# Kernel optimization log

Measured on AMD Instinct MI355X. Metric: run time of the kernel, lower is better.

## Reference

```python
import jax, jax.numpy as jnp
import numpy as np

B, T, C = 2, 2048, 768
H, N_LEFT = 12, 6
D = C // H


def setup_inputs() -> dict:
    key = jax.random.key(0)
    ks = jax.random.split(key, 4)
    x = jax.random.normal(ks[0], (B, T, C), dtype=jnp.float32)
    attention_mask = jnp.ones((B, T), dtype=jnp.int32)
    Wqkv_w = jax.random.normal(ks[1], (3 * C, C), dtype=jnp.float32) * (C ** -0.5)
    Wqkv_b = jnp.zeros((3 * C,), dtype=jnp.float32)
    Wo_w = jax.random.normal(ks[2], (C, C), dtype=jnp.float32) * (C ** -0.5)
    Wo_b = jnp.zeros((C,), dtype=jnp.float32)
    return {"x": x, "attention_mask": attention_mask, "Wqkv_w": Wqkv_w,
            "Wqkv_b": Wqkv_b, "Wo_w": Wo_w, "Wo_b": Wo_b}


def _attend(q, k, v, mask):
    # q,k,v: [B,h,T,D]; mask: [B,1,T,T] additive
    s = jnp.einsum('bhqd,bhkd->bhqk', q, k) * (D ** -0.5) + mask
    a = jax.nn.softmax(s.astype(jnp.float32), axis=-1).astype(q.dtype)
    return jnp.einsum('bhqk,bhkd->bhqd', a, v)


def reference(x, attention_mask, Wqkv_w, Wqkv_b, Wo_w, Wo_b):
    neg = jnp.finfo(x.dtype).min
    # padding mask [B,1,1,T]: 0 where valid, neg where padded
    pad = (1.0 - attention_mask.astype(x.dtype))[:, None, None, :] * neg
    i = jnp.arange(T)
    tri = (i[None, :] > i[:, None]).astype(x.dtype) * neg   # triu(neg, 1)
    left_mask = tri[None, None] + pad                        # causal (look left)
    right_mask = tri.T[None, None] + pad                     # anti-causal (look right)

    qkv = (x @ Wqkv_w.T + Wqkv_b).reshape(B, T, 3, H, D)
    qkv = jnp.transpose(qkv, (0, 3, 2, 1, 4))                # [B,H,3,T,D]
    q, k, v = qkv[:, :, 0], qkv[:, :, 1], qkv[:, :, 2]

    lc = _attend(q[:, :N_LEFT], k[:, :N_LEFT], v[:, :N_LEFT], left_mask)
    rc = _attend(q[:, N_LEFT:], k[:, N_LEFT:], v[:, N_LEFT:], right_mask)
    ctx = jnp.concatenate([lc, rc], axis=1)                  # [B,H,T,D]
    ctx = jnp.transpose(ctx, (0, 2, 1, 3)).reshape(B, T, C)
    out = ctx @ Wo_w.T + Wo_b
    return out
```

## Files before the change

### kernel.cpp

```cpp
#include <hip/hip_runtime.h>


typedef unsigned short u16;
typedef __bf16 bf16x8 __attribute__((ext_vector_type(8)));
typedef float fx4 __attribute__((ext_vector_type(4)));
typedef unsigned short u16x8 __attribute__((ext_vector_type(8)));
typedef unsigned short u16x4 __attribute__((ext_vector_type(4)));
typedef _Float16 hx4 __attribute__((ext_vector_type(4)));
typedef __fp16 fp16x2 __attribute__((ext_vector_type(2)));

#define T_SEQ 2048
#define C_DIM 768
#define NHEAD 12
#define HDIM  64
#define NCHUNK 1152
#define NHEAVY 384
#define LOG2E_8 0.18033688f

__device__ __forceinline__ u16 f2bf(float f) {
  unsigned u = __float_as_uint(f);
  u += 0x7fffu + ((u >> 16) & 1u);
  return (u16)(u >> 16);
}
__device__ __forceinline__ u16 f2h(float f) {
  union { _Float16 h; u16 u; } cv; cv.h = (_Float16)f; return cv.u;
}

__device__ __forceinline__ void gl2lds16(const u16* g, u16* l) {
  __builtin_amdgcn_global_load_lds(
      (const __attribute__((address_space(1))) void*)g,
      (__attribute__((address_space(3))) void*)l, 16, 0, 0);
}

__global__ void cvt_swz_k(const float* __restrict__ x,
                          const float* __restrict__ wqkv,
                          const float* __restrict__ wo,
                          u16* __restrict__ out) {
  int i = blockIdx.x * blockDim.x + threadIdx.x;
  if (i >= 688128) return;
  int m = i / 96;
  int c8 = (i - m * 96) << 3;
  const float* src;
  if (m < 4096)       src = x    + (size_t)m * C_DIM + c8;
  else if (m < 6400)  src = wqkv + (size_t)(m - 4096) * C_DIM + c8;
  else                src = wo   + (size_t)(m - 6400) * C_DIM + c8;
  fx4 a = *(const fx4*)src, b = *(const fx4*)(src + 4);
  u16x8 o;
  #pragma unroll
  for (int j = 0; j < 4; ++j) { o[j] = f2bf(a[j]); o[4 + j] = f2bf(b[j]); }
  *(u16x8*)&out[(size_t)m * C_DIM + (c8 ^ ((m & 7) << 3))] = o;
}

__global__ void maskcvt_k(const int* __restrict__ am, float* __restrict__ mf,
                          unsigned* __restrict__ fbits, int* __restrict__ cnt) {
  int i = blockIdx.x * blockDim.x + threadIdx.x;
  if (i < 4096) mf[i] = am[i] ? 0.f : -1e30f;
  if (blockIdx.x == 16) {
    int t = threadIdx.x;
    if (t == 0) cnt[0] = 0;
    if (t < 64) {
      int bb = t >> 5, kt = t & 31;
      const int* seg = am + (bb << 11) + (kt << 6);
      int anyz = 0;
      for (int j = 0; j < 64; ++j) anyz |= (seg[j] == 0);
      unsigned long long bal = __ballot(anyz != 0);
      if (t == 0)  fbits[0] = (unsigned)(bal & 0xffffffffull);
      if (t == 32) fbits[1] = (unsigned)(bal >> 32);
    }
  }
}

__device__ __forceinline__ void gemm_core_64x128(const u16* __restrict__ A,
                                                 const u16* __restrict__ B,
                                                 int m0, int n0,
                                                 u16* As, u16* Bs,
                                                 fx4 acc[4][2]) {
  const int tid = threadIdx.x;
  const int lane = tid & 63, wv = tid >> 6;
  const int wn = wv << 5;
  const int lr = lane & 15, lg = lane >> 4;
  const int swk = (lr & 7) << 3;
  const int scol = (tid & 7) << 3;
  #pragma unroll
  for (int mt = 0; mt < 4; ++mt)
    #pragma unroll
    for (int nt = 0; nt < 2; ++nt) acc[mt][nt] = fx4{0.f, 0.f, 0.f, 0.f};

  #pragma unroll
  for (int p = 0; p < 2; ++p) {
    int row = (tid >> 3) + (p << 5);
    gl2lds16(&A[(size_t)(m0 + row) * C_DIM + scol], &As[(row << 6) + scol]);
  }
  #pragma unroll
  for (int p = 0; p < 4; ++p) {
    int row = (tid >> 3) + (p << 5);
    gl2lds16(&B[(size_t)(n0 + row) * C_DIM + scol], &Bs[(row << 6) + scol]);
  }

  int buf = 0;
  for (int k0 = 0; k0 < C_DIM; k0 += 64, buf ^= 1) {
    __syncthreads();
    if (k0 + 64 < C_DIM) {
      u16* Ad = &As[(buf ^ 1) << 12];
      u16* Bd = &Bs[(buf ^ 1) << 13];
      #pragma unroll
      for (int p = 0; p < 2; ++p) {
        int row = (tid >> 3) + (p << 5);
        gl2lds16(&A[(size_t)(m0 + row) * C_DIM + k0 + 64 + scol], &Ad[(row << 6) + scol]);
      }
      #pragma unroll
      for (int p = 0; p < 4; ++p) {
        int row = (tid >> 3) + (p << 5);
        gl2lds16(&B[(size_t)(n0 + row) * C_DIM + k0 + 64 + scol], &Bd[(row << 6) + scol]);
      }
    }
    const u16* Ab = &As[buf << 12];
    const u16* Bb = &Bs[buf << 13];
    #pragma unroll
    for (int kk = 0; kk < 64; kk += 32) {
      bf16x8 af[4], bfr[2];
      #pragma unroll
      for (int mt = 0; mt < 4; ++mt)
        af[mt] = *(const bf16x8*)&Ab[((mt * 16 + lr) << 6) + ((kk + lg * 8) ^ swk)];
      #pragma unroll
      for (int nt = 0; nt < 2; ++nt)
        bfr[nt] = *(const bf16x8*)&Bb[((wn + nt * 16 + lr) << 6) + ((kk + lg * 8) ^ swk)];
      #pragma unroll
      for (int mt = 0; mt < 4; ++mt)
        #pragma unroll
        for (int nt = 0; nt < 2; ++nt)
          acc[mt][nt] = __builtin_amdgcn_mfma_f32_16x16x32_bf16(
              af[mt], bfr[nt], acc[mt][nt], 0, 0, 0);
    }
  }
}

__global__ __launch_bounds__(256) void gemm_qkv_k(
    const u16* __restrict__ A, const u16* __restrict__ B,
    const float* __restrict__ bias,
    u16* __restrict__ qb, u16* __restrict__ kswz, u16* __restrict__ vswz) {
  __shared__ __align__(16) u16 As[2][64 * 64];
  __shared__ __align__(16) u16 Bs[2][128 * 64];
  int m0 = blockIdx.y << 6, n0 = blockIdx.x << 7;
  fx4 acc[4][2];
  gemm_core_64x128(A, B, m0, n0, &As[0][0], &Bs[0][0], acc);

  const int tid = threadIdx.x, lane = tid & 63, wv = tid >> 6;
  const int wn = wv << 5;
  const int lr = lane & 15, lg = lane >> 4;
  const int part = n0 / 768;
  const int n0r = n0 - part * 768;
  const int bb = m0 >> 11, kt = (m0 >> 6) & 31;
  u16* Sc = &Bs[0][0];
  __syncthreads();

  if (part < 2) {
    #pragma unroll
    for (int nt = 0; nt < 2; ++nt) {
      int nl = wn + nt * 16 + lr;
      float bv = bias[n0 + nl];
      #pragma unroll
      for (int mt = 0; mt < 4; ++mt) {
        #pragma unroll
        for (int r = 0; r < 4; ++r) {
          int m = mt * 16 + lg * 4 + r;
          Sc[(m << 7) + (nl ^ ((m & 15) << 2))] = f2bf(acc[mt][nt][r] + bv);
        }
      }
    }
    __syncthreads();
    int c4 = (tid & 31) << 2;
    int ng = n0r + c4;
    int h = ng >> 6, d = ng & 63;
    int bh = bb * NHEAD + h;
    #pragma unroll
    for (int p = 0; p < 8; ++p) {
      int m = (tid >> 5) + (p << 3);
      u16x4 v = *(const u16x4*)&Sc[(m << 7) + (c4 ^ ((m & 15) << 2))];
      if (part == 0) {
        int t = (m0 & 2047) + m;
        *(u16x4*)&qb[(((size_t)bh << 11) + t) * HDIM + d] = v;
      } else {
        *(u16x4*)&kswz[((size_t)(bh * 32 + kt) << 12) + (m << 6) +
                       (d ^ ((m & 7) << 3))] = v;
      }
    }
  } else {
    #pragma unroll
    for (int nt = 0; nt < 2; ++nt) {
      int nl = wn + nt * 16 + lr;
      float bv = bias[n0 + nl];
      #pragma unroll
      for (int mt = 0; mt < 4; ++mt) {
        u16x4 pk;
        #pragma unroll
        for (int r = 0; r < 4; ++r) pk[r] = f2h(acc[mt][nt][r] + bv);
        int m4 = (mt << 2) + lg;
        *(u16x4*)&Sc[(nl << 6) + ((m4 ^ (nl & 15)) << 2)] = pk;
      }
    }
    __syncthreads();
    int tr4 = tid & 15;
    #pragma unroll
    for (int p = 0; p < 8; ++p) {
      int nl = (tid >> 4) + (p << 4);
      int ng = n0r + nl;
      int h = ng >> 6, d = ng & 63;
      u16x4 v = *(const u16x4*)&Sc[(nl << 6) + ((tr4 ^ (nl & 15)) << 2)];
      size_t tile = (size_t)((bb * NHEAD + h) * 32 + kt) << 12;
      *(u16x4*)&vswz[tile + (d << 6) + ((tr4 ^ (d & 15)) << 2)] = v;
    }
  }
}

__device__ __forceinline__ void gemm_core_64x64(const u16* __restrict__ A,
                                                const u16* __restrict__ B,
                                                int m0, int n0,
                                                u16* As, u16* Bs,
                                                fx4 acc[2][2]) {
  const int tid = threadIdx.x;
  const int lane = tid & 63, wv = tid >> 6;
  const int wm = (wv & 1) << 5, wn = (wv >> 1) << 5;
  const int lr = lane & 15, lg = lane >> 4;
  const int swk = (lr & 7) << 3;
  const int scol = (tid & 7) << 3;
  #pragma unroll
  for (int mt = 0; mt < 2; ++mt)
    #pragma unroll
    for (int nt = 0; nt < 2; ++nt) acc[mt][nt] = fx4{0.f, 0.f, 0.f, 0.f};

  #pragma unroll
  for (int p = 0; p < 2; ++p) {
    int row = (tid >> 3) + (p << 5);
    gl2lds16(&A[(size_t)(m0 + row) * C_DIM + scol], &As[(row << 6) + scol]);
    gl2lds16(&B[(size_t)(n0 + row) * C_DIM + scol], &Bs[(row << 6) + scol]);
  }

  int buf = 0;
  for (int k0 = 0; k0 < C_DIM; k0 += 64, buf ^= 1) {
    __syncthreads();
    if (k0 + 64 < C_DIM) {
      u16* Ad = &As[(buf ^ 1) << 12];
      u16* Bd = &Bs[(buf ^ 1) << 12];
      #pragma unroll
      for (int p = 0; p < 2; ++p) {
        int row = (tid >> 3) + (p << 5);
        gl2lds16(&A[(size_t)(m0 + row) * C_DIM + k0 + 64 + scol], &Ad[(row << 6) + scol]);
        gl2lds16(&B[(size_t)(n0 + row) * C_DIM + k0 + 64 + scol], &Bd[(row << 6) + scol]);
      }
    }
    const u16* Ab = &As[buf << 12];
    const u16* Bb = &Bs[buf << 12];
    #pragma unroll
    for (int kk = 0; kk < 64; kk += 32) {
      bf16x8 af[2], bfr[2];
      #pragma unroll
      for (int mt = 0; mt < 2; ++mt)
        af[mt] = *(const bf16x8*)&Ab[((wm + mt * 16 + lr) << 6) + ((kk + lg * 8) ^ swk)];
      #pragma unroll
      for (int nt = 0; nt < 2; ++nt)
        bfr[nt] = *(const bf16x8*)&Bb[((wn + nt * 16 + lr) << 6) + ((kk + lg * 8) ^ swk)];
      #pragma unroll
      for (int mt = 0; mt < 2; ++mt)
        #pragma unroll
        for (int nt = 0; nt < 2; ++nt)
          acc[mt][nt] = __builtin_amdgcn_mfma_f32_16x16x32_bf16(
              af[mt], bfr[nt], acc[mt][nt], 0, 0, 0);
    }
  }
}

__global__ __launch_bounds__(256) void gemm_out_k(
    const u16* __restrict__ A, const u16* __restrict__ B,
    const float* __restrict__ bias, float* __restrict__ out) {
  __shared__ __align__(16) u16 As[2][64 * 64];
  __shared__ __align__(16) u16 Bs[2][64 * 64];
  int m0 = blockIdx.y << 6, n0 = blockIdx.x << 6;
  fx4 acc[2][2];
  gemm_core_64x64(A, B, m0, n0, &As[0][0], &Bs[0][0], acc);

  const int tid = threadIdx.x, lane = tid & 63, wv = tid >> 6;
  const int wm = (wv & 1) << 5, wn = (wv >> 1) << 5;
  const int lr = lane & 15, lg = lane >> 4;
  #pragma unroll
  for (int nt = 0; nt < 2; ++nt) {
    int n = n0 + wn + nt * 16 + lr;
    float bv = bias[n];
    #pragma unroll
    for (int mt = 0; mt < 2; ++mt) {
      #pragma unroll
      for (int r = 0; r < 4; ++r) {
        int m = m0 + wm + mt * 16 + lg * 4 + r;
        out[(size_t)m * C_DIM + n] = acc[mt][nt][r] + bv;
      }
    }
  }
}

__global__ __launch_bounds__(256) void attn_k(
    const u16* __restrict__ q, const u16* __restrict__ kswz,
    const u16* __restrict__ vswz, const float* __restrict__ maskf,
    const unsigned* __restrict__ fbits,
    u16* __restrict__ ctx, int* __restrict__ counter,
    float* __restrict__ oacc, float* __restrict__ lacc) {
  __shared__ __align__(16) u16 Ks[2][4096];
  __shared__ __align__(16) u16 Vt[2][4096];
  __shared__ int s_w;

  const int tid = threadIdx.x, lane = tid & 63, wv = tid >> 6;
  const int lr = lane & 15, lg = lane >> 4;
  const int swk = (lr & 7) << 3;
  const int swv = (lr & 15) << 2;
  const int e0 = (lr << 6) + ((lg * 8) ^ swk);
  const int e1 = (lr << 6) + ((32 + lg * 8) ^ swk);
  int ve[4];
  #pragma unroll
  for (int nt = 0; nt < 4; ++nt)
    ve[nt] = (lr << 6) + (((nt << 4) + (lg << 2)) ^ swv);

  for (;;) {
    if (tid == 0) s_w = atomicAdd(counter, 1);
    __syncthreads();
    int w = s_w;
    if (w >= NCHUNK) break;
    int s = w / 24, bh = w - s * 24;
    int bb = bh / NHEAD, h = bh - bb * NHEAD;
    bool causal = (h < 6);
    int qt, kt0, kt1;
    bool direct;
    if (s < 16) {
      direct = false;
      if (causal) { qt = 16 + s; kt0 = 0;  kt1 = 15; }
      else        { qt = s;      kt0 = 16; kt1 = 31; }
    } else {
      int u = s - 16;
      int L = 16 - (u >> 1);
      if ((u & 1) == 0) {
        direct = false;
        if (causal) { qt = L + 15; kt0 = 16; kt1 = qt; }
        else        { qt = 16 - L; kt0 = qt; kt1 = 15; }
      } else {
        direct = true;
        if (causal) { qt = L - 1;  kt0 = 0;  kt1 = qt; }
        else        { qt = 32 - L; kt0 = qt; kt1 = 31; }
      }
    }
    int hv = (bh << 4) + (causal ? qt - 16 : qt);
    size_t tile_base = (size_t)(bh * 32) << 12;
    unsigned fb = fbits[bb];

    {
      const u16* kg = kswz + tile_base + ((size_t)kt0 << 12);
      const u16* vg = vswz + tile_base + ((size_t)kt0 << 12);
      #pragma unroll
      for (int c2 = 0; c2 < 2; ++c2) {
        int e = (wv << 10) + (c2 << 9) + (lane << 3);
        gl2lds16(kg + e, &Ks[0][e]);
        gl2lds16(vg + e, &Vt[0][e]);
      }
    }

    int q0 = qt << 6;
    size_t head_off = ((size_t)bh << 11) * HDIM;
    int qrow = q0 + wv * 16 + lr;
    bf16x8 qf0 = *(const bf16x8*)&q[head_off + (size_t)qrow * HDIM + lg * 8];
    bf16x8 qf1 = *(const bf16x8*)&q[head_off + (size_t)qrow * HDIM + 32 + lg * 8];
    const float* mrow = maskf + (bb << 11);

    fx4 o[4];
    #pragma unroll
    for (int dt = 0; dt < 4; ++dt) o[dt] = fx4{0.f, 0.f, 0.f, 0.f};
    float l_i = 0.f;

    int buf = 0;
    for (int kt = kt0; kt <= kt1; ++kt, buf ^= 1) {
      __syncthreads();
      if (kt < kt1) {
        const u16* kg = kswz + tile_base + ((size_t)(kt + 1) << 12);
        const u16* vg = vswz + tile_base + ((size_t)(kt + 1) << 12);
        #pragma unroll
        for (int c2 = 0; c2 < 2; ++c2) {
          int e = (wv << 10) + (c2 << 9) + (lane << 3);
          gl2lds16(kg + e, &Ks[buf ^ 1][e]);
          gl2lds16(vg + e, &Vt[buf ^ 1][e]);
        }
      }

      const u16* kb = &Ks[buf][0];
      const u16* vbl = &Vt[buf][0];

      fx4 st[4];
      #pragma unroll
      for (int nt = 0; nt < 4; ++nt) {
        bf16x8 kf0 = *(const bf16x8*)&kb[e0 + (nt << 10)];
        bf16x8 kf1 = *(const bf16x8*)&kb[e1 + (nt << 10)];
        fx4 z = fx4{0.f, 0.f, 0.f, 0.f};
        z = __builtin_amdgcn_mfma_f32_16x16x32_bf16(kf0, qf0, z, 0, 0, 0);
        st[nt] = __builtin_amdgcn_mfma_f32_16x16x32_bf16(kf1, qf1, z, 0, 0, 0);
      }

      float ps0 = 0.f, ps1 = 0.f;
      if (kt == qt) {
        #pragma unroll
        for (int nt = 0; nt < 4; ++nt) {
          int kb0 = (kt << 6) + nt * 16 + lg * 4;
          fx4 mv = *(const fx4*)&mrow[kb0];
          #pragma unroll
          for (int r = 0; r < 4; ++r) {
            float arg = st[nt][r] * LOG2E_8 + mv[r];
            int kabs = kb0 + r;
            bool dead = causal ? (kabs > qrow) : (kabs < qrow);
            arg = dead ? -1e30f : arg;
            float p = __builtin_amdgcn_exp2f(arg);
            st[nt][r] = p;
            if (r & 1) ps1 += p; else ps0 += p;
          }
        }
      } else if ((fb >> kt) & 1u) {
        #pragma unroll
        for (int nt = 0; nt < 4; ++nt) {
          int kb0 = (kt << 6) + nt * 16 + lg * 4;
          fx4 mv = *(const fx4*)&mrow[kb0];
          #pragma unroll
          for (int r = 0; r < 4; ++r) {
            float p = __builtin_amdgcn_exp2f(st[nt][r] * LOG2E_8 + mv[r]);
            st[nt][r] = p;
            if (r & 1) ps1 += p; else ps0 += p;
          }
        }
      } else {
        #pragma unroll
        for (int nt = 0; nt < 4; ++nt)
          #pragma unroll
          for (int r = 0; r < 4; ++r) {
            float p = __builtin_amdgcn_exp2f(st[nt][r] * LOG2E_8);
            st[nt][r] = p;
            if (r & 1) ps1 += p; else ps0 += p;
          }
      }
      l_i += ps0 + ps1;

      #pragma unroll
      for (int nt = 0; nt < 4; ++nt) {
        union { hx4 v; fp16x2 hh[2]; } pu;
        pu.hh[0] = __builtin_amdgcn_cvt_pkrtz(st[nt][0], st[nt][1]);
        pu.hh[1] = __builtin_amdgcn_cvt_pkrtz(st[nt][2], st[nt][3]);
        hx4 pf = pu.v;
        #pragma unroll
        for (int dt = 0; dt < 4; ++dt) {
          hx4 vf = *(const hx4*)&vbl[ve[nt] + (dt << 10)];
          o[dt] = __builtin_amdgcn_mfma_f32_16x16x16f16(vf, pf, o[dt], 0, 0, 0);
        }
      }
    }

    l_i += __shfl_xor(l_i, 16, 64);
    l_i += __shfl_xor(l_i, 32, 64);
    if (direct) {
      float inv = 1.f / l_i;
      size_t rowb = ((size_t)(bb << 11) + qrow) * C_DIM;
      int csw = (qrow & 7) << 3;
      #pragma unroll
      for (int dt = 0; dt < 4; ++dt) {
        u16x4 pk;
        #pragma unroll
        for (int r = 0; r < 4; ++r) pk[r] = f2bf(o[dt][r] * inv);
        int colb = h * HDIM + dt * 16 + lg * 4;
        *(u16x4*)&ctx[rowb + (colb ^ csw)] = pk;
      }
    } else {
      float* ob = oacc + ((size_t)hv << 12);
      int qq = wv * 16 + lr;
      #pragma unroll
      for (int dt = 0; dt < 4; ++dt)
        #pragma unroll
        for (int r = 0; r < 4; ++r) {
          int d = dt * 16 + lg * 4 + r;
          atomicAdd(&ob[(d << 6) + qq], o[dt][r]);
        }
      if (lg == 0) atomicAdd(&lacc[(hv << 6) + qq], l_i);
    }
  }
}

__global__ __launch_bounds__(256) void fin_k(const float* __restrict__ oacc,
                                             const float* __restrict__ lacc,
                                             u16* __restrict__ ctx) {
  int hv = blockIdx.x;
  int bh = hv >> 4, idx = hv & 15;
  int bb = bh / NHEAD, h = bh - bb * NHEAD;
  int qt = (h < 6) ? idx + 16 : idx;
  int q0 = qt << 6;
  int tid = threadIdx.x;
  int qq = tid & 63, dblk = tid >> 6;
  const float* ob = oacc + ((size_t)hv << 12);
  float inv = 1.f / lacc[(hv << 6) + qq];
  int tq = q0 + qq;
  size_t rowb = ((size_t)(bb << 11) + tq) * C_DIM;
  int csw = (tq & 7) << 3;
  #pragma unroll
  for (int c = 0; c < 4; ++c) {
    u16x4 pk;
    #pragma unroll
    for (int r = 0; r < 4; ++r) {
      int d = dblk * 16 + c * 4 + r;
      pk[r] = f2bf(ob[(d << 6) + qq] * inv);
    }
    int colb = h * HDIM + dblk * 16 + c * 4;
    *(u16x4*)&ctx[rowb + (colb ^ csw)] = pk;
  }
}

extern "C" void kernel_launch(void* const* d_in, const int* in_sizes, int n_in,
                              void* d_out, int out_size, void* d_ws, size_t ws_size,
                              hipStream_t stream) {
  const float* x     = (const float*)d_in[0];
  const int*   amask = (const int*)d_in[1];
  const float* wqkv  = (const float*)d_in[2];
  const float* bqkv  = (const float*)d_in[3];
  const float* wo    = (const float*)d_in[4];
  const float* bo    = (const float*)d_in[5];
  float* out = (float*)d_out;

  char* ws = (char*)d_ws;
  u16*      xb    = (u16*)(ws + 0);
  u16*      wqkvb = (u16*)(ws + 6291456);
  u16*      wob   = (u16*)(ws + 9830400);
  u16*      qb    = (u16*)(ws + 11010048);
  u16*      kswz  = (u16*)(ws + 17301504);
  u16*      vswz  = (u16*)(ws + 23592960);
  u16*      ctxb  = (u16*)(ws + 29884416);
  float*    maskf = (float*)(ws + 36175872);
  int*      cnt   = (int*)(ws + 36192256);
  unsigned* fbits = (unsigned*)(ws + 36192320);
  float*    oacc  = (float*)(ws + 0);
  float*    lacc  = (float*)(ws + 6291456);

  cvt_swz_k<<<2688, 256, 0, stream>>>(x, wqkv, wo, xb);
  maskcvt_k<<<17, 256, 0, stream>>>(amask, maskf, fbits, cnt);

  gemm_qkv_k<<<dim3(18, 64), 256, 0, stream>>>(xb, wqkvb, bqkv, qb, kswz, vswz);
  hipMemsetAsync(ws, 0, 6291456 + 98304, stream);
  attn_k<<<768, 256, 0, stream>>>(qb, kswz, vswz, maskf, fbits, ctxb, cnt,
                                  oacc, lacc);
  fin_k<<<NHEAVY, 256, 0, stream>>>(oacc, lacc, ctxb);
  gemm_out_k<<<dim3(12, 64), 256, 0, stream>>>(ctxb, wob, bo, out);
}
```

Before: 179.5 us.

## Process 128-row query tiles per workgroup with table-driven split-K scheduling

```diff
diff --git a/kernel.cpp b/kernel.cpp
--- a/kernel.cpp
+++ b/kernel.cpp
@@ -13,9 +13,25 @@
 #define C_DIM 768
 #define NHEAD 12
 #define HDIM  64
-#define NCHUNK 1152
-#define NHEAVY 384
+#define NCHUNK 960
+#define NHEAVY 288
 #define LOG2E_8 0.18033688f
+
+__constant__ unsigned char SLOT_TAB[40] = {
+  15, 31, 47, 63,
+  14, 30, 46,
+  13, 29, 45,
+  12, 28, 44,
+  11, 27, 43,
+  10, 26,
+   9, 25,
+   8, 24,
+   7, 23,
+   6,  5,  4,  3,
+  62, 42, 22,  2,
+  61, 41, 21,  1,
+  60, 40, 20,  0
+};
 
 __device__ __forceinline__ u16 f2bf(float f) {
   unsigned u = __float_as_uint(f);
@@ -297,7 +313,7 @@
   }
 }
 
-__global__ __launch_bounds__(256) void attn_k(
+__global__ __launch_bounds__(256, 3) void attn_k(
     const u16* __restrict__ q, const u16* __restrict__ kswz,
     const u16* __restrict__ vswz, const float* __restrict__ maskf,
     const unsigned* __restrict__ fbits,
@@ -326,26 +342,18 @@
     int s = w / 24, bh = w - s * 24;
     int bb = bh / NHEAD, h = bh - bb * NHEAD;
     bool causal = (h < 6);
-    int qt, kt0, kt1;
-    bool direct;
-    if (s < 16) {
-      direct = false;
-      if (causal) { qt = 16 + s; kt0 = 0;  kt1 = 15; }
-      else        { qt = s;      kt0 = 16; kt1 = 31; }
-    } else {
-      int u = s - 16;
-      int L = 16 - (u >> 1);
-      if ((u & 1) == 0) {
-        direct = false;
-        if (causal) { qt = L + 15; kt0 = 16; kt1 = qt; }
-        else        { qt = 16 - L; kt0 = qt; kt1 = 15; }
-      } else {
-        direct = true;
-        if (causal) { qt = L - 1;  kt0 = 0;  kt1 = qt; }
-        else        { qt = 32 - L; kt0 = qt; kt1 = 31; }
-      }
-    }
-    int hv = (bh << 4) + (causal ? qt - 16 : qt);
+    int tab = SLOT_TAB[s];
+    int it = tab & 15, j = tab >> 4;
+    int wgt = 2 * it + 2;
+    int len = min(8, wgt - 8 * j);
+    bool direct = (it <= 3);
+    int ia = causal ? it : 15 - it;
+    int q0 = ia << 7;
+    int kt0, kt1;
+    if (causal) { kt0 = 8 * j;          kt1 = kt0 + len - 1; }
+    else        { kt1 = 31 - 8 * j;     kt0 = kt1 - len + 1; }
+    int dlo = 2 * ia;
+    int hv = bh * 12 + (causal ? it - 4 : ia);
     size_t tile_base = (size_t)(bh * 32) << 12;
     unsigned fb = fbits[bb];
 
@@ -360,17 +368,20 @@
       }
     }
 
-    int q0 = qt << 6;
     size_t head_off = ((size_t)bh << 11) * HDIM;
-    int qrow = q0 + wv * 16 + lr;
-    bf16x8 qf0 = *(const bf16x8*)&q[head_off + (size_t)qrow * HDIM + lg * 8];
-    bf16x8 qf1 = *(const bf16x8*)&q[head_off + (size_t)qrow * HDIM + 32 + lg * 8];
+    int qrow0 = q0 + (wv << 5) + lr;
+    int qrow1 = qrow0 + 16;
+    bf16x8 qf00 = *(const bf16x8*)&q[head_off + (size_t)qrow0 * HDIM + lg * 8];
+    bf16x8 qf01 = *(const bf16x8*)&q[head_off + (size_t)qrow0 * HDIM + 32 + lg * 8];
+    bf16x8 qf10 = *(const bf16x8*)&q[head_off + (size_t)qrow1 * HDIM + lg * 8];
+    bf16x8 qf11 = *(const bf16x8*)&q[head_off + (size_t)qrow1 * HDIM + 32 + lg * 8];
     const float* mrow = maskf + (bb << 11);
 
-    fx4 o[4];
-    #pragma unroll
-    for (int dt = 0; dt < 4; ++dt) o[dt] = fx4{0.f, 0.f, 0.f, 0.f};
-    float l_i = 0.f;
+    fx4 o0[4], o1[4];
+    #pragma unroll
+    for (int dt = 0; dt < 4; ++dt) { o0[dt] = fx4{0.f,0.f,0.f,0.f};
+                                     o1[dt] = fx4{0.f,0.f,0.f,0.f}; }
+    float l0 = 0.f, l1 = 0.f;
 
     int buf = 0;
     for (int kt = kt0; kt <= kt1; ++kt, buf ^= 1) {
@@ -389,31 +400,40 @@
       const u16* kb = &Ks[buf][0];
       const u16* vbl = &Vt[buf][0];
 
-      fx4 st[4];
+      fx4 st0[4], st1[4];
       #pragma unroll
       for (int nt = 0; nt < 4; ++nt) {
         bf16x8 kf0 = *(const bf16x8*)&kb[e0 + (nt << 10)];
         bf16x8 kf1 = *(const bf16x8*)&kb[e1 + (nt << 10)];
-        fx4 z = fx4{0.f, 0.f, 0.f, 0.f};
-        z = __builtin_amdgcn_mfma_f32_16x16x32_bf16(kf0, qf0, z, 0, 0, 0);
-        st[nt] = __builtin_amdgcn_mfma_f32_16x16x32_bf16(kf1, qf1, z, 0, 0, 0);
-      }
-
-      float ps0 = 0.f, ps1 = 0.f;
-      if (kt == qt) {
+        fx4 z0 = fx4{0.f,0.f,0.f,0.f};
+        z0 = __builtin_amdgcn_mfma_f32_16x16x32_bf16(kf0, qf00, z0, 0, 0, 0);
+        st0[nt] = __builtin_amdgcn_mfma_f32_16x16x32_bf16(kf1, qf01, z0, 0, 0, 0);
+        fx4 z1 = fx4{0.f,0.f,0.f,0.f};
+        z1 = __builtin_amdgcn_mfma_f32_16x16x32_bf16(kf0, qf10, z1, 0, 0, 0);
+        st1[nt] = __builtin_amdgcn_mfma_f32_16x16x32_bf16(kf1, qf11, z1, 0, 0, 0);
+      }
+
+      bool dtile = causal ? (kt >= dlo) : (kt <= dlo + 1);
+      float p00 = 0.f, p01 = 0.f, p10 = 0.f, p11 = 0.f;
+      if (dtile) {
         #pragma unroll
         for (int nt = 0; nt < 4; ++nt) {
           int kb0 = (kt << 6) + nt * 16 + lg * 4;
           fx4 mv = *(const fx4*)&mrow[kb0];
           #pragma unroll
           for (int r = 0; r < 4; ++r) {
-            float arg = st[nt][r] * LOG2E_8 + mv[r];
             int kabs = kb0 + r;
-            bool dead = causal ? (kabs > qrow) : (kabs < qrow);
-            arg = dead ? -1e30f : arg;
-            float p = __builtin_amdgcn_exp2f(arg);
-            st[nt][r] = p;
-            if (r & 1) ps1 += p; else ps0 += p;
+            float a0 = st0[nt][r] * LOG2E_8 + mv[r];
+            float a1 = st1[nt][r] * LOG2E_8 + mv[r];
+            bool d0 = causal ? (kabs > qrow0) : (kabs < qrow0);
+            bool d1 = causal ? (kabs > qrow1) : (kabs < qrow1);
+            a0 = d0 ? -1e30f : a0;
+            a1 = d1 ? -1e30f : a1;
+            float e0p = __builtin_amdgcn_exp2f(a0);
+            float e1p = __builtin_amdgcn_exp2f(a1);
+            st0[nt][r] = e0p; st1[nt][r] = e1p;
+            if (r & 1) { p01 += e0p; p11 += e1p; }
+            else       { p00 += e0p; p10 += e1p; }
           }
         }
       } else if ((fb >> kt) & 1u) {
@@ -423,9 +443,11 @@
           fx4 mv = *(const fx4*)&mrow[kb0];
           #pragma unroll
           for (int r = 0; r < 4; ++r) {
-            float p = __builtin_amdgcn_exp2f(st[nt][r] * LOG2E_8 + mv[r]);
-            st[nt][r] = p;
-            if (r & 1) ps1 += p; else ps0 += p;
+            float e0p = __builtin_amdgcn_exp2f(st0[nt][r] * LOG2E_8 + mv[r]);
+            float e1p = __builtin_amdgcn_exp2f(st1[nt][r] * LOG2E_8 + mv[r]);
+            st0[nt][r] = e0p; st1[nt][r] = e1p;
+            if (r & 1) { p01 += e0p; p11 += e1p; }
+            else       { p00 += e0p; p10 += e1p; }
           }
         }
       } else {
@@ -433,52 +455,69 @@
         for (int nt = 0; nt < 4; ++nt)
           #pragma unroll
           for (int r = 0; r < 4; ++r) {
-            float p = __builtin_amdgcn_exp2f(st[nt][r] * LOG2E_8);
-            st[nt][r] = p;
-            if (r & 1) ps1 += p; else ps0 += p;
+            float e0p = __builtin_amdgcn_exp2f(st0[nt][r] * LOG2E_8);
+            float e1p = __builtin_amdgcn_exp2f(st1[nt][r] * LOG2E_8);
+            st0[nt][r] = e0p; st1[nt][r] = e1p;
+            if (r & 1) { p01 += e0p; p11 += e1p; }
+            else       { p00 += e0p; p10 += e1p; }
           }
       }
-      l_i += ps0 + ps1;
+      l0 += p00 + p01;
+      l1 += p10 + p11;
 
       #pragma unroll
       for (int nt = 0; nt < 4; ++nt) {
-        union { hx4 v; fp16x2 hh[2]; } pu;
-        pu.hh[0] = __builtin_amdgcn_cvt_pkrtz(st[nt][0], st[nt][1]);
-        pu.hh[1] = __builtin_amdgcn_cvt_pkrtz(st[nt][2], st[nt][3]);
-        hx4 pf = pu.v;
+        union { hx4 v; fp16x2 hh[2]; } pu0, pu1;
+        pu0.hh[0] = __builtin_amdgcn_cvt_pkrtz(st0[nt][0], st0[nt][1]);
+        pu0.hh[1] = __builtin_amdgcn_cvt_pkrtz(st0[nt][2], st0[nt][3]);
+        pu1.hh[0] = __builtin_amdgcn_cvt_pkrtz(st1[nt][0], st1[nt][1]);
+        pu1.hh[1] = __builtin_amdgcn_cvt_pkrtz(st1[nt][2], st1[nt][3]);
+        hx4 pf0 = pu0.v, pf1 = pu1.v;
         #pragma unroll
         for (int dt = 0; dt < 4; ++dt) {
           hx4 vf = *(const hx4*)&vbl[ve[nt] + (dt << 10)];
-          o[dt] = __builtin_amdgcn_mfma_f32_16x16x16f16(vf, pf, o[dt], 0, 0, 0);
-        }
-      }
-    }
-
-    l_i += __shfl_xor(l_i, 16, 64);
-    l_i += __shfl_xor(l_i, 32, 64);
+          o0[dt] = __builtin_amdgcn_mfma_f32_16x16x16f16(vf, pf0, o0[dt], 0, 0, 0);
+          o1[dt] = __builtin_amdgcn_mfma_f32_16x16x16f16(vf, pf1, o1[dt], 0, 0, 0);
+        }
+      }
+    }
+
+    l0 += __shfl_xor(l0, 16, 64);
+    l0 += __shfl_xor(l0, 32, 64);
+    l1 += __shfl_xor(l1, 16, 64);
+    l1 += __shfl_xor(l1, 32, 64);
     if (direct) {
-      float inv = 1.f / l_i;
-      size_t rowb = ((size_t)(bb << 11) + qrow) * C_DIM;
-      int csw = (qrow & 7) << 3;
+      float inv0 = 1.f / l0, inv1 = 1.f / l1;
+      size_t rowb0 = ((size_t)(bb << 11) + qrow0) * C_DIM;
+      size_t rowb1 = ((size_t)(bb << 11) + qrow1) * C_DIM;
+      int csw0 = (qrow0 & 7) << 3, csw1 = (qrow1 & 7) << 3;
       #pragma unroll
       for (int dt = 0; dt < 4; ++dt) {
-        u16x4 pk;
-        #pragma unroll
-        for (int r = 0; r < 4; ++r) pk[r] = f2bf(o[dt][r] * inv);
+        u16x4 pk0, pk1;
+        #pragma unroll
+        for (int r = 0; r < 4; ++r) {
+          pk0[r] = f2bf(o0[dt][r] * inv0);
+          pk1[r] = f2bf(o1[dt][r] * inv1);
+        }
         int colb = h * HDIM + dt * 16 + lg * 4;
-        *(u16x4*)&ctx[rowb + (colb ^ csw)] = pk;
+        *(u16x4*)&ctx[rowb0 + (colb ^ csw0)] = pk0;
+        *(u16x4*)&ctx[rowb1 + (colb ^ csw1)] = pk1;
       }
     } else {
-      float* ob = oacc + ((size_t)hv << 12);
-      int qq = wv * 16 + lr;
+      float* ob = oacc + ((size_t)hv << 13);
+      int qq0 = (wv << 5) + lr;
       #pragma unroll
       for (int dt = 0; dt < 4; ++dt)
         #pragma unroll
         for (int r = 0; r < 4; ++r) {
           int d = dt * 16 + lg * 4 + r;
-          atomicAdd(&ob[(d << 6) + qq], o[dt][r]);
-        }
-      if (lg == 0) atomicAdd(&lacc[(hv << 6) + qq], l_i);
+          atomicAdd(&ob[(d << 7) + qq0], o0[dt][r]);
+          atomicAdd(&ob[(d << 7) + qq0 + 16], o1[dt][r]);
+        }
+      if (lg == 0) {
+        atomicAdd(&lacc[(hv << 7) + qq0], l0);
+        atomicAdd(&lacc[(hv << 7) + qq0 + 16], l1);
+      }
     }
   }
 }
@@ -487,26 +526,24 @@
                                              const float* __restrict__ lacc,
                                              u16* __restrict__ ctx) {
   int hv = blockIdx.x;
-  int bh = hv >> 4, idx = hv & 15;
+  int bh = hv / 12, idx = hv - bh * 12;
   int bb = bh / NHEAD, h = bh - bb * NHEAD;
-  int qt = (h < 6) ? idx + 16 : idx;
-  int q0 = qt << 6;
+  int q0 = ((h < 6) ? idx + 4 : idx) << 7;
   int tid = threadIdx.x;
-  int qq = tid & 63, dblk = tid >> 6;
-  const float* ob = oacc + ((size_t)hv << 12);
-  float inv = 1.f / lacc[(hv << 6) + qq];
+  int qq = tid & 127, dh = tid >> 7;
+  const float* ob = oacc + ((size_t)hv << 13);
+  float inv = 1.f / lacc[(hv << 7) + qq];
   int tq = q0 + qq;
   size_t rowb = ((size_t)(bb << 11) + tq) * C_DIM;
   int csw = (tq & 7) << 3;
   #pragma unroll
-  for (int c = 0; c < 4; ++c) {
+  for (int c = 0; c < 8; ++c) {
+    int d = dh * 32 + c * 4;
     u16x4 pk;
     #pragma unroll
-    for (int r = 0; r < 4; ++r) {
-      int d = dblk * 16 + c * 4 + r;
-      pk[r] = f2bf(ob[(d << 6) + qq] * inv);
-    }
-    int colb = h * HDIM + dblk * 16 + c * 4;
+    for (int r = 0; r < 4; ++r)
+      pk[r] = f2bf(ob[((d + r) << 7) + qq] * inv);
+    int colb = h * HDIM + d;
     *(u16x4*)&ctx[rowb + (colb ^ csw)] = pk;
   }
 }
@@ -534,13 +571,13 @@
   int*      cnt   = (int*)(ws + 36192256);
   unsigned* fbits = (unsigned*)(ws + 36192320);
   float*    oacc  = (float*)(ws + 0);
-  float*    lacc  = (float*)(ws + 6291456);
+  float*    lacc  = (float*)(ws + 9437184);
 
   cvt_swz_k<<<2688, 256, 0, stream>>>(x, wqkv, wo, xb);
   maskcvt_k<<<17, 256, 0, stream>>>(amask, maskf, fbits, cnt);
 
   gemm_qkv_k<<<dim3(18, 64), 256, 0, stream>>>(xb, wqkvb, bqkv, qb, kswz, vswz);
-  hipMemsetAsync(ws, 0, 6291456 + 98304, stream);
+  hipMemsetAsync(ws, 0, 9437184 + 147456, stream);
   attn_k<<<768, 256, 0, stream>>>(qb, kswz, vswz, maskf, fbits, ctxb, cnt,
                                   oacc, lacc);
   fin_k<<<NHEAVY, 256, 0, stream>>>(oacc, lacc, ctxb);
```

Measured after the change: 194.1 us. 1.08x slower.
